# Performance work log

Hardware: AMD Instinct MI355X
Metric: run time of the kernel (lower is better)

## Reference

```python
import jax, jax.numpy as jnp
import numpy as np

B, L, H, E = 16, 4096, 3, 512   # q: [B, L, H, E]; in_channels = H*E = 1536
M = 128                          # number of selected frequency modes
F_LEN = L // 2 + 1               # rfft length


def setup_inputs() -> dict:
    key = jax.random.key(0)
    kq, kr, ki = jax.random.split(key, 3)
    q = jax.random.normal(kq, (B, L, H, E), dtype=jnp.float32)
    # get_frequency_modes('random'): shuffle range(L//2), take M, sort (distinct modes)
    rng = np.random.default_rng(0)
    index = jnp.asarray(np.sort(rng.permutation(L // 2)[:M]).astype(np.int32))
    # torch.rand on cfloat samples real & imag uniform[0,1); scale = 1/(in*out)
    scale = 1.0 / float((H * E) * (H * E))
    w_real = scale * jax.random.uniform(kr, (H, E, E, M), dtype=jnp.float32)
    w_imag = scale * jax.random.uniform(ki, (H, E, E, M), dtype=jnp.float32)
    return {"q": q, "w_real": w_real, "w_imag": w_imag, "index": index, "mask": 0}


def reference(q, w_real, w_imag, index, mask):
    # mask is unused by FourierBlock.forward (matches original)
    w = (w_real + 1j * w_imag).astype(jnp.complex64)      # [H, E_in, E_out, M]
    x = jnp.transpose(q, (0, 2, 3, 1))                    # [B, H, E, L]
    x_ft = jnp.fft.rfft(x, axis=-1)                       # [B, H, E, F_LEN] complex64
    # gather selected modes, batched complex matmul over all modes at once
    x_sel = x_ft[..., index]                              # [B, H, E_in, M]
    out_sel = jnp.einsum('bhim,hiom->bhom', x_sel, w)     # [B, H, E_out, M]
    # scatter back into zero-initialized spectrum
    out_ft = jnp.zeros((B, H, E, F_LEN), dtype=jnp.complex64).at[..., index].set(out_sel)
    x_out = jnp.fft.irfft(out_ft, n=L, axis=-1)           # [B, H, E, L] float32
    return x_out
```

## Files before the change

### kernel.cpp

```cpp
#include <hip/hip_runtime.h>
#include <hip/hip_bf16.h>


#define L_TOT 4096

typedef __attribute__((ext_vector_type(4))) float f32x4;
typedef __attribute__((ext_vector_type(2))) float f32x2;
typedef __attribute__((ext_vector_type(2))) unsigned u32x2;
typedef __attribute__((ext_vector_type(8))) short s16x8;
typedef __attribute__((ext_vector_type(4))) unsigned short u16x4;

__device__ __forceinline__ unsigned short f2bf(float f) {
    unsigned u = __builtin_bit_cast(unsigned, f);
    u = (u + 0x7fffu + ((u >> 16) & 1u)) >> 16;
    return (unsigned short)u;
}

__device__ __forceinline__ void gload_lds16(const void* g, void* l) {
    __builtin_amdgcn_global_load_lds((const __attribute__((address_space(1))) void*)g,
                                     (__attribute__((address_space(3))) void*)l,
                                     16, 0, 0);
}

__global__ __launch_bounds__(256) void build_ta(const int* __restrict__ index,
                                                unsigned short* __restrict__ T_A) {
    const int idx = blockIdx.x * 256 + threadIdx.x;
    const int m2 = idx >> 12;
    const int l  = idx & (L_TOT - 1);
    const int k  = index[m2 >> 1];
    const int tt = (k * l) & (L_TOT - 1);
    const float x = (float)tt * (1.0f / 2048.0f);
    T_A[idx] = f2bf((m2 & 1) ? -sinpif(x) : cospif(x));
}

__global__ __launch_bounds__(256) void build_tc(const int* __restrict__ index,
                                                unsigned short* __restrict__ T_C) {
    const int idx = blockIdx.x * 256 + threadIdx.x;
    const int l  = idx >> 8;
    const int m2 = idx & 255;
    const int k  = index[m2 >> 1];
    const int tt = (k * l) & (L_TOT - 1);
    const float x = (float)tt * (1.0f / 2048.0f);
    const float s = (k == 0 ? 1.0f : 2.0f) * (1.0f / (float)L_TOT);
    T_C[idx] = f2bf(s * ((m2 & 1) ? -sinpif(x) : cospif(x)));
}

__global__ __launch_bounds__(256) void gemm_a(const float* __restrict__ q,
                                              const unsigned short* __restrict__ T_A,
                                              unsigned short* __restrict__ Xbf) {
    __shared__ unsigned short As[64 * 64];
    __shared__ unsigned short Bs[256 * 64];

    const int bid = blockIdx.x;
    const int b   = bid / 24;
    const int cht = bid % 24;
    const int ch0 = cht * 64;
    const int h   = ch0 >> 9;
    const int i0  = ch0 & 511;
    const int t   = threadIdx.x;
    const int lane = t & 63;
    const int w    = t >> 6;
    const int chq  = t & 15;
    const int lg   = t >> 4;

    const float* qb = q + (size_t)b * L_TOT * 1536 + ch0 + chq * 4;

    f32x4 acc[4][4];
#pragma unroll
    for (int mi = 0; mi < 4; ++mi)
#pragma unroll
        for (int ni = 0; ni < 4; ++ni) acc[mi][ni] = (f32x4)0.0f;

    for (int kt = 0; kt < L_TOT; kt += 64) {
        __syncthreads();
#pragma unroll
        for (int p = 0; p < 8; ++p) {
            const int u = p * 256 + t;
            const int row = u >> 3, c16 = u & 7;
            const unsigned short* src = T_A + (size_t)row * L_TOT + kt + ((c16 ^ (row & 7)) * 8);
            unsigned short* dst = Bs + (size_t)(p * 256 + w * 64) * 8;
            gload_lds16(src, dst);
        }
        f32x4 v[4];
#pragma unroll
        for (int r = 0; r < 4; ++r)
            v[r] = *reinterpret_cast<const f32x4*>(qb + (size_t)(kt + lg * 4 + r) * 1536);
#pragma unroll
        for (int j = 0; j < 4; ++j) {
            const int c = chq * 4 + j;
            uint2 pk;
            pk.x = f2bf(v[0][j]) | ((unsigned)f2bf(v[1][j]) << 16);
            pk.y = f2bf(v[2][j]) | ((unsigned)f2bf(v[3][j]) << 16);
            *reinterpret_cast<uint2*>(As + c * 64 + ((lg * 4) ^ ((c & 7) << 3))) = pk;
        }
        __syncthreads();

#pragma unroll
        for (int kk = 0; kk < 2; ++kk) {
            const int c16 = kk * 4 + (lane >> 4);
            s16x8 af[4], bfr[4];
#pragma unroll
            for (int mi = 0; mi < 4; ++mi) {
                const int row = mi * 16 + (lane & 15);
                af[mi] = *reinterpret_cast<const s16x8*>(As + row * 64 + ((c16 ^ (row & 7)) * 8));
            }
#pragma unroll
            for (int ni = 0; ni < 4; ++ni) {
                const int row = w * 64 + ni * 16 + (lane & 15);
                bfr[ni] = *reinterpret_cast<const s16x8*>(Bs + row * 64 + ((c16 ^ (row & 7)) * 8));
            }
#pragma unroll
            for (int mi = 0; mi < 4; ++mi)
#pragma unroll
                for (int ni = 0; ni < 4; ++ni)
                    acc[mi][ni] = __builtin_amdgcn_mfma_f32_16x16x32_bf16(af[mi], bfr[ni], acc[mi][ni], 0, 0, 0);
        }
    }

    const size_t cbase = (((size_t)h * 16 + b) * 512 + i0) * 256;
#pragma unroll
    for (int mi = 0; mi < 4; ++mi) {
        const int r0 = mi * 16 + (lane >> 4) * 4;
#pragma unroll
        for (int ni = 0; ni < 4; ++ni) {
            const int col = w * 64 + ni * 16 + (lane & 15);
#pragma unroll
            for (int j = 0; j < 4; ++j)
                Xbf[cbase + (size_t)(r0 + j) * 256 + col] = f2bf(acc[mi][ni][j]);
        }
    }
}

template <int MODE>
__global__ __launch_bounds__(256) void gemm_bf16(const unsigned short* __restrict__ A,
                                                 const unsigned short* __restrict__ Bt,
                                                 void* __restrict__ Cv) {
    constexpr int BM   = 128;
    constexpr int BK   = 64;
    constexpr int KTOT = 256;
    constexpr int LDAB = 256;
    constexpr int LDC  = 4096;
    constexpr int MFR  = BM / 32;
    constexpr int APASS = BM * 8 / 256;
    constexpr int BPASS = 4;

    __shared__ unsigned short As[BM * BK];
    __shared__ unsigned short Bs[128 * BK];

    const int t = threadIdx.x;
    const int lane = t & 63;
    const int w = t >> 6;
    const int wr = w >> 1, wc = w & 1;

    const int mt = blockIdx.x >> 5, nt = blockIdx.x & 31;
    const unsigned short* Ab = A + (size_t)mt * 128 * 256;
    const unsigned short* Bb = Bt + (size_t)nt * 128 * 256;
    const size_t cbase = (size_t)mt * 128 * 4096 + nt * 128;

    f32x4 acc[MFR][4];
#pragma unroll
    for (int mi = 0; mi < MFR; ++mi)
#pragma unroll
        for (int ni = 0; ni < 4; ++ni) acc[mi][ni] = (f32x4)0.0f;

    for (int kt = 0; kt < KTOT; kt += BK) {
        __syncthreads();
#pragma unroll
        for (int p = 0; p < APASS; ++p) {
            const int u = p * 256 + t;
            const int row = u >> 3, c16 = u & 7;
            const unsigned short* src = Ab + (size_t)row * LDAB + kt + ((c16 ^ (row & 7)) * 8);
            unsigned short* dst = As + (size_t)(p * 256 + w * 64) * 8;
            gload_lds16(src, dst);
        }
#pragma unroll
        for (int p = 0; p < BPASS; ++p) {
            const int u = p * 256 + t;
            const int row = u >> 3, c16 = u & 7;
            const unsigned short* src = Bb + (size_t)row * LDAB + kt + ((c16 ^ (row & 7)) * 8);
            unsigned short* dst = Bs + (size_t)(p * 256 + w * 64) * 8;
            gload_lds16(src, dst);
        }
        __syncthreads();

#pragma unroll
        for (int kk = 0; kk < 2; ++kk) {
            const int c16 = kk * 4 + (lane >> 4);
            s16x8 af[MFR], bfr[4];
#pragma unroll
            for (int mi = 0; mi < MFR; ++mi) {
                const int row = wr * (BM / 2) + mi * 16 + (lane & 15);
                af[mi] = *reinterpret_cast<const s16x8*>(As + row * BK + ((c16 ^ (row & 7)) * 8));
            }
#pragma unroll
            for (int ni = 0; ni < 4; ++ni) {
                const int row = wc * 64 + ni * 16 + (lane & 15);
                bfr[ni] = *reinterpret_cast<const s16x8*>(Bs + row * BK + ((c16 ^ (row & 7)) * 8));
            }
#pragma unroll
            for (int mi = 0; mi < MFR; ++mi)
#pragma unroll
                for (int ni = 0; ni < 4; ++ni)
                    acc[mi][ni] = __builtin_amdgcn_mfma_f32_16x16x32_bf16(af[mi], bfr[ni], acc[mi][ni], 0, 0, 0);
        }
    }

#pragma unroll
    for (int mi = 0; mi < MFR; ++mi) {
        const int r0 = wr * (BM / 2) + mi * 16 + (lane >> 4) * 4;
#pragma unroll
        for (int ni = 0; ni < 4; ++ni) {
            const int col = wc * 64 + ni * 16 + (lane & 15);
#pragma unroll
            for (int j = 0; j < 4; ++j)
                ((float*)Cv)[cbase + (size_t)(r0 + j) * LDC + col] = acc[mi][ni][j];
        }
    }
}

#define SB_STAGE(BUF, IB)                                                      \
    _Pragma("unroll")                                                          \
    for (int p = 0; p < 2; ++p) {                                              \
        const int u = p * 256 + t;                                             \
        const int row = u >> 5;                                                \
        const int col = u & 31;                                                \
        const int ii = row >> 2, oo = row & 3;                                 \
        const size_t goff = (size_t)((IB) + ii) * 65536 + oo * 128 + col * 4;  \
        gload_lds16(wr_base + goff, (char*)&Wl[BUF][0][0][0][0] + (size_t)u * 16); \
        gload_lds16(wi_base + goff, (char*)&Wl[BUF][1][0][0][0] + (size_t)u * 16); \
    }

__global__ __launch_bounds__(256, 3) void stage_b(const unsigned short* __restrict__ Xbf,
                                                  const float* __restrict__ wr,
                                                  const float* __restrict__ wi,
                                                  unsigned short* __restrict__ Y0,
                                                  unsigned short* __restrict__ P1) {
    __shared__ float Wl[2][2][4][4][128];
    const int bid = blockIdx.x;
    const int ic  = bid / 384;
    const int g   = bid % 384;
    const int h   = g >> 7;
    const int ot  = g & 127;
    const int t    = threadIdx.x;
    const int lane = t & 63;
    const int w    = t >> 6;
    const int b0   = w * 4;
    const int o0   = ot * 4;
    const int i_lo = ic * 256;

    const float* wr_base = wr + (size_t)h * 33554432 + (size_t)o0 * 128;
    const float* wi_base = wi + (size_t)h * 33554432 + (size_t)o0 * 128;
    const unsigned short* x0 = Xbf + (size_t)(h * 16 + b0) * 512 * 256 + lane * 4;

    float aR[4][4][2], aI[4][4][2];
#pragma unroll
    for (int bb = 0; bb < 4; ++bb)
#pragma unroll
        for (int oo = 0; oo < 4; ++oo) {
            aR[bb][oo][0] = aR[bb][oo][1] = 0.f;
            aI[bb][oo][0] = aI[bb][oo][1] = 0.f;
        }

    SB_STAGE(0, i_lo);
    __syncthreads();

    int cur = 0;
#pragma unroll 1
    for (int c = 0; c < 64; ++c) {
        const int ib = i_lo + c * 4;
        if (c + 1 < 64) {
            if (cur == 0) { SB_STAGE(1, ib + 4); }
            else          { SB_STAGE(0, ib + 4); }
        }
#pragma unroll
        for (int i = 0; i < 4; ++i) {
            u32x2 xv[4];
#pragma unroll
            for (int bb = 0; bb < 4; ++bb)
                xv[bb] = *reinterpret_cast<const u32x2*>(x0 + (size_t)bb * 131072 + (size_t)(ib + i) * 256);
            f32x2 wrv[4], wiv[4];
#pragma unroll
            for (int oo = 0; oo < 4; ++oo) {
                wrv[oo] = *reinterpret_cast<const f32x2*>(&Wl[cur][0][i][oo][lane * 2]);
                wiv[oo] = *reinterpret_cast<const f32x2*>(&Wl[cur][1][i][oo][lane * 2]);
            }
#pragma unroll
            for (int bb = 0; bb < 4; ++bb) {
                float xr[2], xi[2];
#pragma unroll
                for (int mm = 0; mm < 2; ++mm) {
                    const unsigned xu = xv[bb][mm];
                    xr[mm] = __builtin_bit_cast(float, xu << 16);
                    xi[mm] = __builtin_bit_cast(float, xu & 0xffff0000u);
                }
#pragma unroll
                for (int oo = 0; oo < 4; ++oo)
#pragma unroll
                    for (int mm = 0; mm < 2; ++mm) {
                        const float wrj = wrv[oo][mm];
                        const float wij = wiv[oo][mm];
                        aR[bb][oo][mm] = fmaf(xr[mm], wrj, aR[bb][oo][mm]);
                        aR[bb][oo][mm] = fmaf(-xi[mm], wij, aR[bb][oo][mm]);
                        aI[bb][oo][mm] = fmaf(xr[mm], wij, aI[bb][oo][mm]);
                        aI[bb][oo][mm] = fmaf(xi[mm], wrj, aI[bb][oo][mm]);
                    }
            }
        }
        __syncthreads();
        cur ^= 1;
    }

    unsigned short* yout = ic ? P1 : Y0;
#pragma unroll
    for (int bb = 0; bb < 4; ++bb)
#pragma unroll
        for (int oo = 0; oo < 4; ++oo) {
            const size_t row = ((size_t)(b0 + bb) * 3 + h) * 512 + o0 + oo;
            u32x2 pk;
            pk.x = f2bf(aR[bb][oo][0]) | ((unsigned)f2bf(aI[bb][oo][0]) << 16);
            pk.y = f2bf(aR[bb][oo][1]) | ((unsigned)f2bf(aI[bb][oo][1]) << 16);
            *reinterpret_cast<u32x2*>(reinterpret_cast<char*>(yout) + row * 512 + lane * 8) = pk;
        }
}

__global__ __launch_bounds__(256) void reduce_y(unsigned short* __restrict__ Ybf,
                                                const unsigned short* __restrict__ P1) {
    const int idx = blockIdx.x * 256 + threadIdx.x;
    const uint4 a = reinterpret_cast<const uint4*>(Ybf)[idx];
    const uint4 b = reinterpret_cast<const uint4*>(P1)[idx];
    const unsigned av[4] = {a.x, a.y, a.z, a.w};
    const unsigned bv[4] = {b.x, b.y, b.z, b.w};
    unsigned rv[4];
#pragma unroll
    for (int j = 0; j < 4; ++j) {
        const float xr = __builtin_bit_cast(float, av[j] << 16);
        const float xi = __builtin_bit_cast(float, av[j] & 0xffff0000u);
        const float yr = __builtin_bit_cast(float, bv[j] << 16);
        const float yi = __builtin_bit_cast(float, bv[j] & 0xffff0000u);
        rv[j] = f2bf(xr + yr) | ((unsigned)f2bf(xi + yi) << 16);
    }
    uint4 r;
    r.x = rv[0]; r.y = rv[1]; r.z = rv[2]; r.w = rv[3];
    reinterpret_cast<uint4*>(Ybf)[idx] = r;
}

extern "C" void kernel_launch(void* const* d_in, const int* in_sizes, int n_in,
                              void* d_out, int out_size, void* d_ws, size_t ws_size,
                              hipStream_t stream) {
    const float* q     = (const float*)d_in[0];
    const float* w_re  = (const float*)d_in[1];
    const float* w_im  = (const float*)d_in[2];
    const int*   index = (const int*)d_in[3];

    char* ws = (char*)d_ws;
    unsigned short* Xbf = (unsigned short*)(ws);
    unsigned short* P1  = (unsigned short*)(ws + 12582912);
    unsigned short* Ybf = (unsigned short*)(ws + 25165824);
    unsigned short* T_A = (unsigned short*)(ws + 37748736);
    unsigned short* T_C = (unsigned short*)(ws + 39845888);

    build_ta<<<4096, 256, 0, stream>>>(index, T_A);
    build_tc<<<4096, 256, 0, stream>>>(index, T_C);
    gemm_a<<<384, 256, 0, stream>>>(q, T_A, Xbf);
    stage_b<<<768, 256, 0, stream>>>(Xbf, w_re, w_im, Ybf, P1);
    reduce_y<<<3072, 256, 0, stream>>>(Ybf, P1);
    gemm_bf16<1><<<6144, 256, 0, stream>>>(Ybf, T_C, (void*)d_out);
}
```

Measured before the change: 476.6 us.

## Hoist X loads and pipeline weight staging with explicit vmcnt waits in stage_b

Restructures the stage_b main loop so that all 16 X loads for a chunk are issued up front, followed by the async LDS weight staging for the next chunk. A partial s_waitcnt vmcnt(20) then waits only for the current buffer's data before a raw s_barrier, in place of __syncthreads. The aim is more memory-level parallelism and less stalling on full waitcnt drains, at the cost of more registers and reliance on hand-counted vmcnt values. On the last iteration it issues a redundant prefetch so the wait count stays uniform.

```diff
diff --git a/kernel.cpp b/kernel.cpp
--- a/kernel.cpp
+++ b/kernel.cpp
@@ -220,8 +220,8 @@
 
 #define SB_STAGE(BUF, IB)                                                      \
     _Pragma("unroll")                                                          \
-    for (int p = 0; p < 2; ++p) {                                              \
-        const int u = p * 256 + t;                                             \
+    for (int pp = 0; pp < 2; ++pp) {                                           \
+        const int u = pp * 256 + t;                                            \
         const int row = u >> 5;                                                \
         const int col = u & 31;                                                \
         const int ii = row >> 2, oo = row & 3;                                 \
@@ -262,34 +262,41 @@
         }
 
     SB_STAGE(0, i_lo);
-    __syncthreads();
-
-    int cur = 0;
+
 #pragma unroll 1
     for (int c = 0; c < 64; ++c) {
         const int ib = i_lo + c * 4;
-        if (c + 1 < 64) {
-            if (cur == 0) { SB_STAGE(1, ib + 4); }
-            else          { SB_STAGE(0, ib + 4); }
-        }
+        const int p  = c & 1;
+        __builtin_amdgcn_sched_barrier(0);
+        u32x2 xv[4][4];
+#pragma unroll
+        for (int i = 0; i < 4; ++i)
+#pragma unroll
+            for (int bb = 0; bb < 4; ++bb)
+                xv[i][bb] = *reinterpret_cast<const u32x2*>(
+                    x0 + (size_t)bb * 131072 + (size_t)(ib + i) * 256);
+        __builtin_amdgcn_sched_barrier(0);
+        const int ibn = (c + 1 < 64) ? (ib + 4) : i_lo;
+        if (p == 0) { SB_STAGE(1, ibn); } else { SB_STAGE(0, ibn); }
+        __builtin_amdgcn_sched_barrier(0);
+        asm volatile("s_waitcnt vmcnt(20)" ::: "memory");
+        __builtin_amdgcn_sched_barrier(0);
+        __builtin_amdgcn_s_barrier();
+        __builtin_amdgcn_sched_barrier(0);
 #pragma unroll
         for (int i = 0; i < 4; ++i) {
-            u32x2 xv[4];
-#pragma unroll
-            for (int bb = 0; bb < 4; ++bb)
-                xv[bb] = *reinterpret_cast<const u32x2*>(x0 + (size_t)bb * 131072 + (size_t)(ib + i) * 256);
             f32x2 wrv[4], wiv[4];
 #pragma unroll
             for (int oo = 0; oo < 4; ++oo) {
-                wrv[oo] = *reinterpret_cast<const f32x2*>(&Wl[cur][0][i][oo][lane * 2]);
-                wiv[oo] = *reinterpret_cast<const f32x2*>(&Wl[cur][1][i][oo][lane * 2]);
+                wrv[oo] = *reinterpret_cast<const f32x2*>(&Wl[p][0][i][oo][lane * 2]);
+                wiv[oo] = *reinterpret_cast<const f32x2*>(&Wl[p][1][i][oo][lane * 2]);
             }
 #pragma unroll
             for (int bb = 0; bb < 4; ++bb) {
                 float xr[2], xi[2];
 #pragma unroll
                 for (int mm = 0; mm < 2; ++mm) {
-                    const unsigned xu = xv[bb][mm];
+                    const unsigned xu = xv[i][bb][mm];
                     xr[mm] = __builtin_bit_cast(float, xu << 16);
                     xi[mm] = __builtin_bit_cast(float, xu & 0xffff0000u);
                 }
@@ -306,8 +313,8 @@
                     }
             }
         }
-        __syncthreads();
-        cur ^= 1;
+        __builtin_amdgcn_sched_barrier(0);
+        __builtin_amdgcn_s_barrier();
     }
 
     unsigned short* yout = ic ? P1 : Y0;
```

After: 478.1 us. Within noise of the previous version (+0.3%).
